# Kernel tuning notes

Measured on AMD Instinct MI355X. Metric: run time of the kernel, lower is better.

Reference implementation:

```python
import jax, jax.numpy as jnp
import numpy as np

NHEAD = 16
D_MODEL = 1024
HEAD_DIM = D_MODEL // NHEAD


def setup_inputs() -> dict:
    key = jax.random.key(0)
    k1, k2, k3 = jax.random.split(key, 3)
    x = jax.random.normal(k1, (4, 2048, D_MODEL), dtype=jnp.float32)
    # lecun_normal-like scaling for stability
    w_qkv = jax.random.normal(k2, (D_MODEL, 3 * D_MODEL), dtype=jnp.float32) / np.sqrt(D_MODEL)
    w_out = jax.random.normal(k3, (D_MODEL, D_MODEL), dtype=jnp.float32) / np.sqrt(D_MODEL)
    return {"x": x, "w_qkv": w_qkv, "w_out": w_out}


def reference(x, w_qkv, w_out):
    # Fused QKV projection (self-attention: x_kv = x)
    qkv = x @ w_qkv  # [B, S, 3*D]
    q, k, v = jnp.split(qkv, 3, axis=-1)
    B, S = x.shape[0], x.shape[1]
    # [B, S, H, hd] -> [B, H, S, hd]
    q = jnp.moveaxis(q.reshape(B, S, NHEAD, HEAD_DIM), -2, -3)
    k = jnp.moveaxis(k.reshape(B, S, NHEAD, HEAD_DIM), -2, -3)
    v = jnp.moveaxis(v.reshape(B, S, NHEAD, HEAD_DIM), -2, -3)
    scale = 1.0 / jnp.sqrt(jnp.float32(HEAD_DIM))
    logits = jnp.einsum('bhqd,bhkd->bhqk', q, k) * scale
    weights = jax.nn.softmax(logits, axis=-1)
    out = jnp.einsum('bhqk,bhkd->bhqd', weights, v)  # [B, H, S, hd]
    out = jnp.moveaxis(out, -3, -2).reshape(B, S, D_MODEL)
    return out @ w_out
```

## Files before the change

kernel.cpp:

```cpp
#include <hip/hip_runtime.h>
#include <hip/hip_bf16.h>
#include <math.h>

#define D_MODEL 1024
#define NHEAD   16
#define HEAD_DIM 64
#define BATCH   4
#define SEQ     2048

typedef __attribute__((ext_vector_type(8))) short bf16x8;
typedef __attribute__((ext_vector_type(4))) float f32x4;

__device__ inline ushort f2bf(float f) {
  __hip_bfloat16 h = __float2bfloat16(f);
  return *reinterpret_cast<ushort*>(&h);
}
__device__ inline uint pk2(float a, float b) {
  return (uint)f2bf(a) | ((uint)f2bf(b) << 16);
}
__device__ inline float bf2f(ushort u) {
  return __uint_as_float((uint)u << 16);
}
__device__ inline void gld_lds16(const ushort* g, ushort* l) {
  __builtin_amdgcn_global_load_lds(
      (const __attribute__((address_space(1))) void*)g,
      (__attribute__((address_space(3))) void*)l, 16, 0, 0);
}

__global__ __launch_bounds__(256) void fill_f32(float* __restrict__ p, int n, float v) {
  int i = blockIdx.x * 256 + threadIdx.x;
  if (i < n) p[i] = v;
}

__global__ __launch_bounds__(256) void cast_bf16(const float* __restrict__ in,
                                                 ushort* __restrict__ out, int n8) {
  int i = blockIdx.x * 256 + threadIdx.x;
  if (i >= n8) return;
  const float4* p = (const float4*)(in + i * 8);
  float4 a = p[0], b = p[1];
  uint4 o;
  o.x = pk2(a.x, a.y); o.y = pk2(a.z, a.w);
  o.z = pk2(b.x, b.y); o.w = pk2(b.z, b.w);
  ((uint4*)out)[i] = o;
}

__global__ __launch_bounds__(256) void transpose_f32_bf16(const float* __restrict__ in,
                                                          ushort* __restrict__ out,
                                                          int R, int C) {
  __shared__ float tile[32][33];
  int tx = threadIdx.x, ty = threadIdx.y;
  int c0 = blockIdx.x * 32, r0 = blockIdx.y * 32;
#pragma unroll
  for (int k = 0; k < 4; ++k)
    tile[ty + 8 * k][tx] = in[(size_t)(r0 + ty + 8 * k) * C + c0 + tx];
  __syncthreads();
#pragma unroll
  for (int k = 0; k < 4; ++k)
    out[(size_t)(c0 + ty + 8 * k) * R + r0 + tx] = f2bf(tile[tx][ty + 8 * k]);
}

template <typename OutT>
__global__ __launch_bounds__(256) void gemm_mfma(const ushort* __restrict__ A,
                                                 const ushort* __restrict__ BT,
                                                 OutT* __restrict__ C,
                                                 int M, int N, int K) {
  __shared__ ushort As[128 * 32];
  __shared__ ushort Bs[128 * 32];

  const int tid = threadIdx.x;
  const int w = tid >> 6, lane = tid & 63;
  const int quad = lane >> 4, l16 = lane & 15;

  int bx = blockIdx.x, by = blockIdx.y;
  {
    int nwg = gridDim.x * gridDim.y;
    if ((nwg & 7) == 0) {
      int bid = by * gridDim.x + bx;
      int chunk = nwg >> 3;
      bid = (bid & 7) * chunk + (bid >> 3);
      bx = bid % gridDim.x;
      by = bid / gridDim.x;
    }
  }
  const int m0 = by * 128, n0 = bx * 128;
  const int wm = (w & 1) * 64, wn = (w >> 1) * 64;

  f32x4 acc[4][4];
#pragma unroll
  for (int mt = 0; mt < 4; ++mt)
#pragma unroll
    for (int nt = 0; nt < 4; ++nt) acc[mt][nt] = (f32x4){0.f, 0.f, 0.f, 0.f};

  const int c0 = w * 64 + lane;
  const int r0a = c0 >> 2, k0a = (c0 & 3) * 8;
  const int c1 = 256 + c0;
  const int r1a = c1 >> 2, k1a = (c1 & 3) * 8;
  const ushort* a_src0 = A + (size_t)(m0 + r0a) * K + k0a;
  const ushort* a_src1 = A + (size_t)(m0 + r1a) * K + k1a;
  const ushort* b_src0 = BT + (size_t)(n0 + r0a) * K + k0a;
  const ushort* b_src1 = BT + (size_t)(n0 + r1a) * K + k1a;
  ushort* a_dst0 = As + (size_t)w * 512;
  ushort* a_dst1 = As + 2048 + (size_t)w * 512;
  ushort* b_dst0 = Bs + (size_t)w * 512;
  ushort* b_dst1 = Bs + 2048 + (size_t)w * 512;

  for (int k0 = 0; k0 < K; k0 += 32) {
    gld_lds16(a_src0 + k0, a_dst0);
    gld_lds16(a_src1 + k0, a_dst1);
    gld_lds16(b_src0 + k0, b_dst0);
    gld_lds16(b_src1 + k0, b_dst1);
    __syncthreads();

    bf16x8 af[4], bf[4];
#pragma unroll
    for (int mt = 0; mt < 4; ++mt)
      af[mt] = *(const bf16x8*)(As + (wm + mt * 16 + l16) * 32 + quad * 8);
#pragma unroll
    for (int nt = 0; nt < 4; ++nt)
      bf[nt] = *(const bf16x8*)(Bs + (wn + nt * 16 + l16) * 32 + quad * 8);
#pragma unroll
    for (int mt = 0; mt < 4; ++mt)
#pragma unroll
      for (int nt = 0; nt < 4; ++nt)
        acc[mt][nt] = __builtin_amdgcn_mfma_f32_16x16x32_bf16(af[mt], bf[nt], acc[mt][nt], 0, 0, 0);
    __syncthreads();
  }

#pragma unroll
  for (int mt = 0; mt < 4; ++mt) {
#pragma unroll
    for (int nt = 0; nt < 4; ++nt) {
#pragma unroll
      for (int r = 0; r < 4; ++r) {
        size_t idx = (size_t)(m0 + wm + mt * 16 + quad * 4 + r) * N + n0 + wn + nt * 16 + l16;
        if constexpr (sizeof(OutT) == 4) C[idx] = acc[mt][nt][r];
        else                             C[idx] = f2bf(acc[mt][nt][r]);
      }
    }
  }
}

#define KST 72
#define VST 72
#define PST 72
__global__ __launch_bounds__(256, 4) void attn_mfma(const ushort* __restrict__ qkv,
                                                    ushort* __restrict__ attn_o) {
  __shared__ ushort Ks[64 * KST];
  __shared__ ushort VTs[64 * VST];
  __shared__ ushort Ps[4 * 32 * PST];

  const int tid = threadIdx.x;
  const int w = tid >> 6, lane = tid & 63;
  const int quad = lane >> 4, l16 = lane & 15;
  const int b = blockIdx.z, h = blockIdx.y, qb = blockIdx.x;
  const int q0 = qb * 128;

  const float qscale = 0.125f * 1.44269504088896f;
  bf16x8 qfrag[2][2];
#pragma unroll
  for (int s = 0; s < 2; ++s) {
    const ushort* qrow = qkv + (size_t)(b * SEQ + q0 + w * 32 + s * 16 + l16) * 3072 + h * 64;
#pragma unroll
    for (int cc = 0; cc < 2; ++cc) {
      bf16x8 f = *(const bf16x8*)(qrow + cc * 32 + quad * 8);
#pragma unroll
      for (int j = 0; j < 8; ++j)
        f[j] = (short)f2bf(bf2f((ushort)f[j]) * qscale);
      qfrag[s][cc] = f;
    }
  }

  f32x4 oacc[2][4], lacc[2];
#pragma unroll
  for (int s = 0; s < 2; ++s) {
#pragma unroll
    for (int i = 0; i < 4; ++i) oacc[s][i] = (f32x4){0.f, 0.f, 0.f, 0.f};
    lacc[s] = (f32x4){0.f, 0.f, 0.f, 0.f};
  }

  bf16x8 ones;
#pragma unroll
  for (int j = 0; j < 8; ++j) ones[j] = (short)0x3F80;

  const int sr = tid >> 2, sc = tid & 3;
  const int kp = tid & 31, dg = tid >> 5;

  ushort* Pw = Ps + w * 32 * PST;

  for (int kt = 0; kt < SEQ / 64; ++kt) {
    {
      const ushort* ksrc = qkv + (size_t)(b * SEQ + kt * 64 + sr) * 3072 + 1024 + h * 64 + sc * 16;
      uint4* kdst = (uint4*)(Ks + sr * KST + sc * 16);
      kdst[0] = ((const uint4*)ksrc)[0];
      kdst[1] = ((const uint4*)ksrc)[1];
    }
    {
      const ushort* v0 = qkv + (size_t)(b * SEQ + kt * 64 + 2 * kp) * 3072 + 2048 + h * 64 + dg * 8;
      const ushort* v1 = v0 + 3072;
      uint4 a = *(const uint4*)v0;
      uint4 c = *(const uint4*)v1;
      const ushort* ae = (const ushort*)&a;
      const ushort* ce = (const ushort*)&c;
#pragma unroll
      for (int j = 0; j < 8; ++j) {
        uint pr = (uint)ae[j] | ((uint)ce[j] << 16);
        *(uint*)(VTs + (dg * 8 + j) * VST + 2 * kp) = pr;
      }
    }
    __syncthreads();

    f32x4 sacc[2][4];
#pragma unroll
    for (int s = 0; s < 2; ++s)
#pragma unroll
      for (int kb = 0; kb < 4; ++kb) sacc[s][kb] = (f32x4){0.f, 0.f, 0.f, 0.f};
    __builtin_amdgcn_s_setprio(1);
#pragma unroll
    for (int kb = 0; kb < 4; ++kb) {
#pragma unroll
      for (int cc = 0; cc < 2; ++cc) {
        bf16x8 kf = *(const bf16x8*)(Ks + (kb * 16 + l16) * KST + cc * 32 + quad * 8);
        sacc[0][kb] = __builtin_amdgcn_mfma_f32_16x16x32_bf16(kf, qfrag[0][cc], sacc[0][kb], 0, 0, 0);
        sacc[1][kb] = __builtin_amdgcn_mfma_f32_16x16x32_bf16(kf, qfrag[1][cc], sacc[1][kb], 0, 0, 0);
      }
    }
    __builtin_amdgcn_s_setprio(0);

#pragma unroll
    for (int s = 0; s < 2; ++s) {
      ushort* prow = Pw + (s * 16 + l16) * PST;
#pragma unroll
      for (int kb = 0; kb < 4; ++kb) {
        uint2 pr;
        pr.x = pk2(exp2f(sacc[s][kb][0]), exp2f(sacc[s][kb][1]));
        pr.y = pk2(exp2f(sacc[s][kb][2]), exp2f(sacc[s][kb][3]));
        *(uint2*)(prow + kb * 16 + quad * 4) = pr;
      }
    }

    __builtin_amdgcn_s_setprio(1);
#pragma unroll
    for (int cc = 0; cc < 2; ++cc) {
      bf16x8 pf0 = *(const bf16x8*)(Pw + l16 * PST + cc * 32 + quad * 8);
      bf16x8 pf1 = *(const bf16x8*)(Pw + (16 + l16) * PST + cc * 32 + quad * 8);
#pragma unroll
      for (int db = 0; db < 4; ++db) {
        bf16x8 vf = *(const bf16x8*)(VTs + (db * 16 + l16) * VST + cc * 32 + quad * 8);
        oacc[0][db] = __builtin_amdgcn_mfma_f32_16x16x32_bf16(pf0, vf, oacc[0][db], 0, 0, 0);
        oacc[1][db] = __builtin_amdgcn_mfma_f32_16x16x32_bf16(pf1, vf, oacc[1][db], 0, 0, 0);
      }
      lacc[0] = __builtin_amdgcn_mfma_f32_16x16x32_bf16(pf0, ones, lacc[0], 0, 0, 0);
      lacc[1] = __builtin_amdgcn_mfma_f32_16x16x32_bf16(pf1, ones, lacc[1], 0, 0, 0);
    }
    __builtin_amdgcn_s_setprio(0);
    __syncthreads();
  }

#pragma unroll
  for (int s = 0; s < 2; ++s) {
    float inv[4];
#pragma unroll
    for (int r = 0; r < 4; ++r) inv[r] = 1.0f / lacc[s][r];
    ushort* orow = attn_o + (size_t)(b * SEQ + q0 + w * 32 + s * 16) * 1024 + h * 64;
#pragma unroll
    for (int db = 0; db < 4; ++db)
#pragma unroll
      for (int r = 0; r < 4; ++r)
        orow[(size_t)(quad * 4 + r) * 1024 + db * 16 + l16] = f2bf(oacc[s][db][r] * inv[r]);
  }
}

extern "C" void kernel_launch(void* const* d_in, const int* in_sizes, int n_in,
                              void* d_out, int out_size, void* d_ws, size_t ws_size,
                              hipStream_t stream) {
  bool ok_n  = (n_in == 3);
  bool ok_s0 = ok_n && (in_sizes[0] == 4 * 2048 * 1024);
  bool ok_s1 = ok_n && (in_sizes[1] == 1024 * 3072);
  bool ok_s2 = ok_n && (in_sizes[2] == 1024 * 1024);
  bool ok_o  = (out_size == 4 * 2048 * 1024);
  bool ok_w  = (ws_size >= (size_t)8192 * 3072 * 4);
  if (!(ok_n && ok_s0 && ok_s1 && ok_s2 && ok_o && ok_w)) {
    float c = 64.0f + 1.0f * ok_n + 2.0f * ok_s0 + 4.0f * ok_s1 +
              8.0f * ok_s2 + 16.0f * ok_o + 32.0f * ok_w;
    fill_f32<<<(out_size + 255) / 256, 256, 0, stream>>>((float*)d_out, out_size, c);
    return;
  }

  const float* x     = (const float*)d_in[0];
  const float* w_qkv = (const float*)d_in[1];
  const float* w_out = (const float*)d_in[2];

  char* ws = (char*)d_ws;
  ushort* qkv    = (ushort*)ws;
  ushort* xb     = (ushort*)(ws + (size_t)48 * 1024 * 1024);
  ushort* attn_o = (ushort*)(ws + (size_t)64 * 1024 * 1024);
  ushort* wqkvT  = (ushort*)(ws + (size_t)80 * 1024 * 1024);
  ushort* woutT  = (ushort*)(ws + (size_t)86 * 1024 * 1024);

  cast_bf16<<<dim3(8192 * 1024 / 8 / 256), dim3(256), 0, stream>>>(x, xb, 8192 * 1024 / 8);
  transpose_f32_bf16<<<dim3(3072 / 32, 1024 / 32), dim3(32, 8), 0, stream>>>(w_qkv, wqkvT, 1024, 3072);
  transpose_f32_bf16<<<dim3(1024 / 32, 1024 / 32), dim3(32, 8), 0, stream>>>(w_out, woutT, 1024, 1024);

  gemm_mfma<ushort><<<dim3(3072 / 128, 8192 / 128), dim3(256), 0, stream>>>(
      xb, wqkvT, qkv, 8192, 3072, 1024);

  attn_mfma<<<dim3(SEQ / 128, NHEAD, BATCH), dim3(256), 0, stream>>>(qkv, attn_o);

  gemm_mfma<float><<<dim3(1024 / 128, 8192 / 128), dim3(256), 0, stream>>>(
      attn_o, woutT, (float*)d_out, 8192, 1024, 1024);
}
```

Measured before the change: 306.8 us.

## Switch attention to 32x32 MFMA, keep P in registers, prefetch next K/V tile

Rewrites the attention inner loop to use 32x32x16 bf16 MFMAs. The S-to-P conversion now stays in registers, using v_permlane32_swap to rearrange exp'd scores directly into A-operand fragments, so the per-wave P shared-memory buffer and its store/load round trip are gone. The next K/V tile is also prefetched into registers during the PV compute, hiding global load latency. In exchange, register pressure rises from the 16-wide accumulators and prefetch registers, which could hurt occupancy at the 4-block launch bound.

```diff
diff --git a/kernel.cpp b/kernel.cpp
--- a/kernel.cpp
+++ b/kernel.cpp
@@ -10,6 +10,7 @@
 
 typedef __attribute__((ext_vector_type(8))) short bf16x8;
 typedef __attribute__((ext_vector_type(4))) float f32x4;
+typedef __attribute__((ext_vector_type(16))) float f32x16;
 
 __device__ inline ushort f2bf(float f) {
   __hip_bfloat16 h = __float2bfloat16(f);
@@ -20,6 +21,12 @@
 }
 __device__ inline float bf2f(ushort u) {
   return __uint_as_float((uint)u << 16);
+}
+__device__ inline f32x16 zero16() {
+  f32x16 z;
+#pragma unroll
+  for (int i = 0; i < 16; ++i) z[i] = 0.f;
+  return z;
 }
 __device__ inline void gld_lds16(const ushort* g, ushort* l) {
   __builtin_amdgcn_global_load_lds(
@@ -142,41 +149,32 @@
 
 #define KST 72
 #define VST 72
-#define PST 72
 __global__ __launch_bounds__(256, 4) void attn_mfma(const ushort* __restrict__ qkv,
                                                     ushort* __restrict__ attn_o) {
   __shared__ ushort Ks[64 * KST];
   __shared__ ushort VTs[64 * VST];
-  __shared__ ushort Ps[4 * 32 * PST];
 
   const int tid = threadIdx.x;
   const int w = tid >> 6, lane = tid & 63;
-  const int quad = lane >> 4, l16 = lane & 15;
+  const int q32 = lane & 31, hi = lane >> 5;
   const int b = blockIdx.z, h = blockIdx.y, qb = blockIdx.x;
   const int q0 = qb * 128;
 
   const float qscale = 0.125f * 1.44269504088896f;
-  bf16x8 qfrag[2][2];
-#pragma unroll
-  for (int s = 0; s < 2; ++s) {
-    const ushort* qrow = qkv + (size_t)(b * SEQ + q0 + w * 32 + s * 16 + l16) * 3072 + h * 64;
-#pragma unroll
-    for (int cc = 0; cc < 2; ++cc) {
-      bf16x8 f = *(const bf16x8*)(qrow + cc * 32 + quad * 8);
+  bf16x8 qfrag[4];
+  {
+    const ushort* qrow = qkv + (size_t)(b * SEQ + q0 + w * 32 + q32) * 3072 + h * 64;
+#pragma unroll
+    for (int dd = 0; dd < 4; ++dd) {
+      bf16x8 f = *(const bf16x8*)(qrow + dd * 16 + hi * 8);
 #pragma unroll
       for (int j = 0; j < 8; ++j)
         f[j] = (short)f2bf(bf2f((ushort)f[j]) * qscale);
-      qfrag[s][cc] = f;
-    }
-  }
-
-  f32x4 oacc[2][4], lacc[2];
-#pragma unroll
-  for (int s = 0; s < 2; ++s) {
-#pragma unroll
-    for (int i = 0; i < 4; ++i) oacc[s][i] = (f32x4){0.f, 0.f, 0.f, 0.f};
-    lacc[s] = (f32x4){0.f, 0.f, 0.f, 0.f};
-  }
+      qfrag[dd] = f;
+    }
+  }
+
+  f32x16 oacc0 = zero16(), oacc1 = zero16(), lacc = zero16();
 
   bf16x8 ones;
 #pragma unroll
@@ -185,88 +183,90 @@
   const int sr = tid >> 2, sc = tid & 3;
   const int kp = tid & 31, dg = tid >> 5;
 
-  ushort* Pw = Ps + w * 32 * PST;
+  const size_t kstep = (size_t)64 * 3072;
+  const ushort* kbase = qkv + (size_t)(b * SEQ + sr) * 3072 + 1024 + h * 64 + sc * 16;
+  const ushort* vbase = qkv + (size_t)(b * SEQ + 2 * kp) * 3072 + 2048 + h * 64 + dg * 8;
+
+  uint4 kreg0, kreg1, vreg0, vreg1;
+  {
+    const uint4* ks = (const uint4*)kbase;
+    kreg0 = ks[0]; kreg1 = ks[1];
+    vreg0 = *(const uint4*)vbase;
+    vreg1 = *(const uint4*)(vbase + 3072);
+  }
 
   for (int kt = 0; kt < SEQ / 64; ++kt) {
     {
-      const ushort* ksrc = qkv + (size_t)(b * SEQ + kt * 64 + sr) * 3072 + 1024 + h * 64 + sc * 16;
       uint4* kdst = (uint4*)(Ks + sr * KST + sc * 16);
-      kdst[0] = ((const uint4*)ksrc)[0];
-      kdst[1] = ((const uint4*)ksrc)[1];
-    }
+      kdst[0] = kreg0; kdst[1] = kreg1;
+      const ushort* ae = (const ushort*)&vreg0;
+      const ushort* ce = (const ushort*)&vreg1;
+#pragma unroll
+      for (int j = 0; j < 8; ++j)
+        *(uint*)(VTs + (dg * 8 + j) * VST + 2 * kp) = (uint)ae[j] | ((uint)ce[j] << 16);
+    }
+    __syncthreads();
+
+    bf16x8 pa[4];
+#pragma unroll
+    for (int kblk = 0; kblk < 2; ++kblk) {
+      f32x16 sacc = zero16();
+      __builtin_amdgcn_s_setprio(1);
+#pragma unroll
+      for (int dd = 0; dd < 4; ++dd) {
+        bf16x8 kf = *(const bf16x8*)(Ks + (kblk * 32 + q32) * KST + dd * 16 + hi * 8);
+        sacc = __builtin_amdgcn_mfma_f32_32x32x16_bf16(kf, qfrag[dd], sacc, 0, 0, 0);
+      }
+      __builtin_amdgcn_s_setprio(0);
+
+      uint d0[4], d1[4];
+#pragma unroll
+      for (int p = 0; p < 4; ++p) {
+        d0[p] = pk2(exp2f(sacc[4 * p + 0]), exp2f(sacc[4 * p + 1]));
+        d1[p] = pk2(exp2f(sacc[4 * p + 2]), exp2f(sacc[4 * p + 3]));
+      }
+#pragma unroll
+      for (int k2 = 0; k2 < 2; ++k2) {
+        uint A0 = d0[2 * k2], B0 = d0[2 * k2 + 1];
+        uint A1 = d1[2 * k2], B1 = d1[2 * k2 + 1];
+        asm("v_permlane32_swap_b32 %0, %1" : "+v"(A0), "+v"(B0));
+        asm("v_permlane32_swap_b32 %0, %1" : "+v"(A1), "+v"(B1));
+        uint4 fr = {A0, A1, B0, B1};
+        pa[kblk * 2 + k2] = *(bf16x8*)&fr;
+        lacc = __builtin_amdgcn_mfma_f32_32x32x16_bf16(pa[kblk * 2 + k2], ones, lacc, 0, 0, 0);
+      }
+    }
+
     {
-      const ushort* v0 = qkv + (size_t)(b * SEQ + kt * 64 + 2 * kp) * 3072 + 2048 + h * 64 + dg * 8;
-      const ushort* v1 = v0 + 3072;
-      uint4 a = *(const uint4*)v0;
-      uint4 c = *(const uint4*)v1;
-      const ushort* ae = (const ushort*)&a;
-      const ushort* ce = (const ushort*)&c;
-#pragma unroll
-      for (int j = 0; j < 8; ++j) {
-        uint pr = (uint)ae[j] | ((uint)ce[j] << 16);
-        *(uint*)(VTs + (dg * 8 + j) * VST + 2 * kp) = pr;
-      }
-    }
-    __syncthreads();
-
-    f32x4 sacc[2][4];
-#pragma unroll
-    for (int s = 0; s < 2; ++s)
-#pragma unroll
-      for (int kb = 0; kb < 4; ++kb) sacc[s][kb] = (f32x4){0.f, 0.f, 0.f, 0.f};
+      int ktn = (kt + 1) & (SEQ / 64 - 1);
+      const uint4* ks = (const uint4*)(kbase + ktn * kstep);
+      kreg0 = ks[0]; kreg1 = ks[1];
+      vreg0 = *(const uint4*)(vbase + ktn * kstep);
+      vreg1 = *(const uint4*)(vbase + ktn * kstep + 3072);
+    }
+
     __builtin_amdgcn_s_setprio(1);
 #pragma unroll
-    for (int kb = 0; kb < 4; ++kb) {
-#pragma unroll
-      for (int cc = 0; cc < 2; ++cc) {
-        bf16x8 kf = *(const bf16x8*)(Ks + (kb * 16 + l16) * KST + cc * 32 + quad * 8);
-        sacc[0][kb] = __builtin_amdgcn_mfma_f32_16x16x32_bf16(kf, qfrag[0][cc], sacc[0][kb], 0, 0, 0);
-        sacc[1][kb] = __builtin_amdgcn_mfma_f32_16x16x32_bf16(kf, qfrag[1][cc], sacc[1][kb], 0, 0, 0);
-      }
-    }
-    __builtin_amdgcn_s_setprio(0);
-
-#pragma unroll
-    for (int s = 0; s < 2; ++s) {
-      ushort* prow = Pw + (s * 16 + l16) * PST;
-#pragma unroll
-      for (int kb = 0; kb < 4; ++kb) {
-        uint2 pr;
-        pr.x = pk2(exp2f(sacc[s][kb][0]), exp2f(sacc[s][kb][1]));
-        pr.y = pk2(exp2f(sacc[s][kb][2]), exp2f(sacc[s][kb][3]));
-        *(uint2*)(prow + kb * 16 + quad * 4) = pr;
-      }
-    }
-
-    __builtin_amdgcn_s_setprio(1);
-#pragma unroll
-    for (int cc = 0; cc < 2; ++cc) {
-      bf16x8 pf0 = *(const bf16x8*)(Pw + l16 * PST + cc * 32 + quad * 8);
-      bf16x8 pf1 = *(const bf16x8*)(Pw + (16 + l16) * PST + cc * 32 + quad * 8);
-#pragma unroll
-      for (int db = 0; db < 4; ++db) {
-        bf16x8 vf = *(const bf16x8*)(VTs + (db * 16 + l16) * VST + cc * 32 + quad * 8);
-        oacc[0][db] = __builtin_amdgcn_mfma_f32_16x16x32_bf16(pf0, vf, oacc[0][db], 0, 0, 0);
-        oacc[1][db] = __builtin_amdgcn_mfma_f32_16x16x32_bf16(pf1, vf, oacc[1][db], 0, 0, 0);
-      }
-      lacc[0] = __builtin_amdgcn_mfma_f32_16x16x32_bf16(pf0, ones, lacc[0], 0, 0, 0);
-      lacc[1] = __builtin_amdgcn_mfma_f32_16x16x32_bf16(pf1, ones, lacc[1], 0, 0, 0);
+    for (int kb2 = 0; kb2 < 4; ++kb2) {
+      bf16x8 vf0 = *(const bf16x8*)(VTs + (q32)*VST + kb2 * 16 + hi * 8);
+      bf16x8 vf1 = *(const bf16x8*)(VTs + (32 + q32) * VST + kb2 * 16 + hi * 8);
+      oacc0 = __builtin_amdgcn_mfma_f32_32x32x16_bf16(pa[kb2], vf0, oacc0, 0, 0, 0);
+      oacc1 = __builtin_amdgcn_mfma_f32_32x32x16_bf16(pa[kb2], vf1, oacc1, 0, 0, 0);
     }
     __builtin_amdgcn_s_setprio(0);
     __syncthreads();
   }
 
 #pragma unroll
-  for (int s = 0; s < 2; ++s) {
-    float inv[4];
-#pragma unroll
-    for (int r = 0; r < 4; ++r) inv[r] = 1.0f / lacc[s][r];
-    ushort* orow = attn_o + (size_t)(b * SEQ + q0 + w * 32 + s * 16) * 1024 + h * 64;
-#pragma unroll
-    for (int db = 0; db < 4; ++db)
-#pragma unroll
-      for (int r = 0; r < 4; ++r)
-        orow[(size_t)(quad * 4 + r) * 1024 + db * 16 + l16] = f2bf(oacc[s][db][r] * inv[r]);
+  for (int p = 0; p < 4; ++p) {
+#pragma unroll
+    for (int r = 0; r < 4; ++r) {
+      int qrow = r + 8 * p + 4 * hi;
+      float linv = 1.0f / lacc[4 * p + r];
+      ushort* orow = attn_o + (size_t)(b * SEQ + q0 + w * 32 + qrow) * 1024 + h * 64 + q32;
+      orow[0]  = f2bf(oacc0[4 * p + r] * linv);
+      orow[32] = f2bf(oacc1[4 * p + r] * linv);
+    }
   }
 }
 
```

After: 307.6 us. Within noise of the previous version (+0.3%).
